# Kernel optimization log

Hardware: AMD Instinct MI355X
Metric: run time of the kernel (lower is better)

## Reference

```python
import jax, jax.numpy as jnp
import numpy as np

N, M, FDIM, EDIM, H, HEADS = 8192, 8192, 128, 128, 64, 4
NEG = -1e9


def setup_inputs() -> dict:
    key = jax.random.key(0)
    ks = jax.random.split(key, 6)
    F0 = jax.random.normal(ks[0], (N, FDIM), dtype=jnp.float32)
    E0 = jax.random.normal(ks[1], (M, EDIM), dtype=jnp.float32)
    A = jax.random.randint(ks[2], (N, M), 0, 2, dtype=jnp.int32)
    Wf = jax.random.normal(ks[3], (HEADS, FDIM, H), dtype=jnp.float32) * 0.05
    We = jax.random.normal(ks[4], (HEADS, EDIM, H), dtype=jnp.float32) * 0.05
    a = jax.random.normal(ks[5], (HEADS, H), dtype=jnp.float32) * 0.05
    return {"F0": F0, "E0": E0, "A": A, "Wf": Wf, "We": We, "a": a}


def reference(F0, E0, A, Wf, We, a):
    # Per-head linear projections: h=head, n/m=nodes, d=hidden
    F1 = jnp.einsum('nf,hfd->hnd', F0, Wf)   # [H, N, D]
    E1 = jnp.einsum('me,hed->hmd', E0, We)   # [H, M, D]
    # Additive GAT scores: (h_src @ a) + (h_dst @ a), broadcast over the grid
    e_src = jnp.einsum('hnd,hd->hn', F1, a)  # [H, N]
    e_dst = jnp.einsum('hmd,hd->hm', E1, a)  # [H, M]
    e = jax.nn.leaky_relu(e_src[:, :, None] + e_dst[:, None, :], negative_slope=0.2)
    e = jnp.where(A[None, :, :] > 0, e, NEG)
    alpha = jax.nn.softmax(e, axis=-1)       # [H, N, M]
    h_prime = jnp.einsum('hnm,hmd->hnd', alpha, E1)  # [H, N, D]
    out = jnp.mean(h_prime, axis=0)          # mean over heads -> [N, D]
    return jax.nn.softmax(out, axis=-1)
```

## Files before the change

### kernel.cpp

```cpp
#include <hip/hip_runtime.h>
#include <hip/hip_fp16.h>

#define NN 8192
#define MM 8192
#define FD 128
#define EDm 128
#define HD 64
#define NH 4
#define NTILE 32

typedef float f32x4 __attribute__((ext_vector_type(4)));
typedef _Float16 h16x8 __attribute__((ext_vector_type(8)));
typedef unsigned int u32;
typedef unsigned long long u64;

__global__ void k_esrc(const float* __restrict__ F0, const float* __restrict__ Wf,
                       const float* __restrict__ a, float* __restrict__ esrc) {
  __shared__ float vfL[NH * FD];
  int t = threadIdx.x;
#pragma unroll
  for (int r = 0; r < 2; ++r) {
    int idx = t + r * 256;
    int h = idx >> 7, f = idx & 127;
    const float* w = Wf + (size_t)(h * FD + f) * HD;
    const float* av = a + h * HD;
    float s = 0.f;
#pragma unroll
    for (int d = 0; d < HD; ++d) s += w[d] * av[d];
    vfL[idx] = s;
  }
  __syncthreads();
  int g = blockIdx.x * 256 + t;
  int n = g >> 2, h = g & 3;
  const float4* fr = (const float4*)(F0 + (size_t)n * FD);
  const float4* vr = (const float4*)(vfL + h * FD);
  float s = 0.f;
#pragma unroll
  for (int i = 0; i < FD / 4; ++i) {
    float4 x = fr[i], y = vr[i];
    s += x.x * y.x + x.y * y.y + x.z * y.z + x.w * y.w;
  }
  esrc[h * NN + n] = s;
}

__global__ void k_e1(const float* __restrict__ E0, const float* __restrict__ We,
                     const float* __restrict__ a, uint4* __restrict__ Bp,
                     _Float16* __restrict__ edh, _Float16* __restrict__ ed2h) {
  int wid = (blockIdx.x * blockDim.x + threadIdx.x) >> 6;
  int lane = threadIdx.x & 63;
  int h = wid >> 10;
  int mg = wid & 1023;
  int m = mg * 8;
  const float* we = We + (size_t)h * EDm * HD + lane;
  const float* e0r = E0 + (size_t)m * EDm;
  float ac[8] = {};
#pragma unroll 4
  for (int e = 0; e < EDm; ++e) {
    float wv = we[e * HD];
#pragma unroll
    for (int j = 0; j < 8; ++j) ac[j] += e0r[j * EDm + e] * wv;
  }
  int mc = mg >> 2, quad = mg & 3, dt = lane >> 4, col = lane & 15;
  union { h16x8 v; uint4 u; } hv;
#pragma unroll
  for (int j = 0; j < 8; ++j) hv.v[j] = (_Float16)ac[j];
  Bp[(((size_t)h * 256 + mc) * 4 + dt) * 64 + quad * 16 + col] = hv.u;

  float av = a[h * HD + lane];
  float d[8];
#pragma unroll
  for (int j = 0; j < 8; ++j) d[j] = ac[j] * av;
#pragma unroll
  for (int o = 32; o; o >>= 1)
#pragma unroll
    for (int j = 0; j < 8; ++j) d[j] += __shfl_xor(d[j], o);
  if (lane == 0) {
    const float L2E = 1.4426950408889634f;
    union { h16x8 v; uint4 u; } e1, e2;
#pragma unroll
    for (int j = 0; j < 8; ++j) {
      e1.v[j] = (_Float16)exp2f(d[j] * L2E);
      e2.v[j] = (_Float16)exp2f(0.2f * d[j] * L2E);
    }
    *(uint4*)(edh + (size_t)h * MM + m) = e1.u;
    *(uint4*)(ed2h + (size_t)h * MM + m) = e2.u;
  }
}

__global__ void k_pack(const int* __restrict__ A, u32* __restrict__ bitsG) {
  const int wid = (blockIdx.x * blockDim.x + threadIdx.x) >> 6;
  const int lane = threadIdx.x & 63;
  const int* ap = A + (size_t)wid * MM + lane;
  u32* op = bitsG + (size_t)wid * 256;
#pragma unroll 2
  for (int c = 0; c < 128; c += 8) {
    int v[8];
#pragma unroll
    for (int k = 0; k < 8; ++k)
      v[k] = __builtin_nontemporal_load(ap + (c + k) * 64);
    u64 b[8];
#pragma unroll
    for (int k = 0; k < 8; ++k) b[k] = __ballot(v[k] > 0);
    if (lane == 0) {
#pragma unroll
      for (int k = 0; k < 8; k += 2) {
        uint4 w = {(u32)b[k], (u32)(b[k] >> 32), (u32)b[k + 1], (u32)(b[k + 1] >> 32)};
        *(uint4*)(op + 2 * (c + k)) = w;
      }
    }
  }
}

__device__ __forceinline__ u32 hm2b(u32 w, int bit) {
  return (((w >> bit) & 1u) | (((w >> (bit + 1)) & 1u) << 16)) * 0xffffu;
}

__global__ __launch_bounds__(1024, 4) void k_main(
    const u32* __restrict__ bitsG, const uint4* __restrict__ Bp,
    const float* __restrict__ esrc, const _Float16* __restrict__ edh,
    const _Float16* __restrict__ ed2h, float* __restrict__ out) {
  __shared__ __align__(16) char smem[41472];
  u32* bits = (u32*)smem;
  float* Hsum = (float*)smem;
  float* Dsum = (float*)(smem + 32768);
  float* hp = (float*)(smem + 33280);

  const int t = threadIdx.x;
  const int lane = t & 63;
  const int wv = t >> 6;
  const int h = wv & 3;
  const int q = wv >> 2;
  const int col = lane & 15;
  const int quad = lane >> 4;
  const int qs = quad * 8;
  const int n0 = blockIdx.x * NTILE;
  const float L2E = 1.4426950408889634f;

#pragma unroll
  for (int i = 0; i < 2; ++i) {
    int tid = t + i * 1024;
    int row = tid >> 6, w4 = tid & 63;
    uint4 v = *(const uint4*)(bitsG + (size_t)(n0 + row) * 256 + w4 * 4);
    *(uint4*)(bits + row * 260 + w4 * 4) = v;
  }

  float s0 = esrc[h * NN + n0 + col];
  float s1 = esrc[h * NN + n0 + 16 + col];
  _Float16 e80 = (_Float16)exp2f(0.8f * s0 * L2E);
  _Float16 e81 = (_Float16)exp2f(0.8f * s1 * L2E);
  h16x8 es80 = {e80, e80, e80, e80, e80, e80, e80, e80};
  h16x8 es81 = {e81, e81, e81, e81, e81, e81, e81, e81};
  const h16x8 ones = {(_Float16)1.f, (_Float16)1.f, (_Float16)1.f, (_Float16)1.f,
                      (_Float16)1.f, (_Float16)1.f, (_Float16)1.f, (_Float16)1.f};

  const _Float16* edp = edh + (size_t)h * MM + qs;
  const _Float16* e2p = ed2h + (size_t)h * MM + qs;
  const uint4* bp = Bp + (size_t)h * 65536 + lane;

  uint4 b0s[2], b1s[2], b2s[2], b3s[2];
  h16x8 eds[2], e2s[2];
  u32 aw0s[2], aw1s[2];
#pragma unroll
  for (int i = 0; i < 2; ++i) {
    size_t w = (size_t)(q * 64 + i);
    b0s[i] = bp[w * 256];
    b1s[i] = bp[w * 256 + 64];
    b2s[i] = bp[w * 256 + 128];
    b3s[i] = bp[w * 256 + 192];
    eds[i] = *(const h16x8*)(edp + w * 32);
    e2s[i] = *(const h16x8*)(e2p + w * 32);
  }
  __syncthreads();

  const u32* rd0 = bits + col * 260 + q * 64;
  const u32* rd1 = bits + (col + 16) * 260 + q * 64;
  aw0s[0] = rd0[0]; aw1s[0] = rd1[0];
  aw0s[1] = rd0[1]; aw1s[1] = rd1[1];

  f32x4 acc[2][4] = {};
  f32x4 accd[2] = {};

#pragma unroll 2
  for (int it = 0; it < 64; ++it) {
    const int s = it & 1;
    const u32 aw0 = aw0s[s], aw1 = aw1s[s];
    union { h16x8 v; uint4 u; } w0, w1, b0, b1, b2, b3;
    b0.u = b0s[s]; b1.u = b1s[s]; b2.u = b2s[s]; b3.u = b3s[s];
    const h16x8 edv = eds[s], e2v = e2s[s];

    int ip = it + 2; if (ip > 63) ip = 63;
    const size_t wn = (size_t)(q * 64 + ip);
    b0s[s] = bp[wn * 256];
    b1s[s] = bp[wn * 256 + 64];
    b2s[s] = bp[wn * 256 + 128];
    b3s[s] = bp[wn * 256 + 192];
    eds[s] = *(const h16x8*)(edp + wn * 32);
    e2s[s] = *(const h16x8*)(e2p + wn * 32);
    aw0s[s] = rd0[ip];
    aw1s[s] = rd1[ip];

    uint4 m0, m1;
    m0.x = hm2b(aw0, qs);     m0.y = hm2b(aw0, qs + 2);
    m0.z = hm2b(aw0, qs + 4); m0.w = hm2b(aw0, qs + 6);
    m1.x = hm2b(aw1, qs);     m1.y = hm2b(aw1, qs + 2);
    m1.z = hm2b(aw1, qs + 4); m1.w = hm2b(aw1, qs + 6);

    w0.v = __builtin_elementwise_max(edv * es80, e2v);
    w1.v = __builtin_elementwise_max(edv * es81, e2v);
    w0.u.x &= m0.x; w0.u.y &= m0.y; w0.u.z &= m0.z; w0.u.w &= m0.w;
    w1.u.x &= m1.x; w1.u.y &= m1.y; w1.u.z &= m1.z; w1.u.w &= m1.w;

    acc[0][0] = __builtin_amdgcn_mfma_f32_16x16x32_f16(w0.v, b0.v, acc[0][0], 0, 0, 0);
    acc[1][0] = __builtin_amdgcn_mfma_f32_16x16x32_f16(w1.v, b0.v, acc[1][0], 0, 0, 0);
    acc[0][1] = __builtin_amdgcn_mfma_f32_16x16x32_f16(w0.v, b1.v, acc[0][1], 0, 0, 0);
    acc[1][1] = __builtin_amdgcn_mfma_f32_16x16x32_f16(w1.v, b1.v, acc[1][1], 0, 0, 0);
    acc[0][2] = __builtin_amdgcn_mfma_f32_16x16x32_f16(w0.v, b2.v, acc[0][2], 0, 0, 0);
    acc[1][2] = __builtin_amdgcn_mfma_f32_16x16x32_f16(w1.v, b2.v, acc[1][2], 0, 0, 0);
    acc[0][3] = __builtin_amdgcn_mfma_f32_16x16x32_f16(w0.v, b3.v, acc[0][3], 0, 0, 0);
    acc[1][3] = __builtin_amdgcn_mfma_f32_16x16x32_f16(w1.v, b3.v, acc[1][3], 0, 0, 0);
    accd[0] = __builtin_amdgcn_mfma_f32_16x16x32_f16(w0.v, ones, accd[0], 0, 0, 0);
    accd[1] = __builtin_amdgcn_mfma_f32_16x16x32_f16(w1.v, ones, accd[1], 0, 0, 0);
  }
  __syncthreads();

  for (int i = t; i < 8320; i += 1024) Hsum[i] = 0.f;
  __syncthreads();

  float* Hh = Hsum + h * 2048;
#pragma unroll
  for (int rt = 0; rt < 2; ++rt) {
#pragma unroll
    for (int dt = 0; dt < 4; ++dt)
#pragma unroll
      for (int r2 = 0; r2 < 4; ++r2)
        atomicAdd(&Hh[(rt * 16 + quad * 4 + r2) * 64 + dt * 16 + col],
                  acc[rt][dt][r2]);
    if (col == 0) {
#pragma unroll
      for (int r2 = 0; r2 < 4; ++r2)
        atomicAdd(&Dsum[h * 32 + rt * 16 + quad * 4 + r2], accd[rt][r2]);
    }
  }
  __syncthreads();

  for (int i = t; i < 2048; i += 1024) {
    int r = i >> 6;
    float v = 0.f;
#pragma unroll
    for (int hh = 0; hh < 4; ++hh) v += Hsum[hh * 2048 + i] / Dsum[hh * 32 + r];
    hp[i] = 0.25f * v;
  }
  __syncthreads();

#pragma unroll
  for (int i = 0; i < 2; ++i) {
    int r = wv * 2 + i;
    float v = hp[r * 64 + lane];
    float mx = v;
#pragma unroll
    for (int o = 32; o; o >>= 1) mx = fmaxf(mx, __shfl_xor(mx, o));
    float p = exp2f((v - mx) * L2E);
    float sm = p;
#pragma unroll
    for (int o = 32; o; o >>= 1) sm += __shfl_xor(sm, o);
    out[(size_t)(n0 + r) * HD + lane] = p / sm;
  }
}

extern "C" void kernel_launch(void* const* d_in, const int* in_sizes, int n_in,
                              void* d_out, int out_size, void* d_ws, size_t ws_size,
                              hipStream_t stream) {
  const float* F0 = (const float*)d_in[0];
  const float* E0 = (const float*)d_in[1];
  const int* A = (const int*)d_in[2];
  const float* Wf = (const float*)d_in[3];
  const float* We = (const float*)d_in[4];
  const float* a = (const float*)d_in[5];
  float* out = (float*)d_out;

  char* w = (char*)d_ws;
  float* esrc = (float*)w;        w += (size_t)NH * NN * 4;
  _Float16* edh = (_Float16*)w;   w += (size_t)NH * MM * 2;
  _Float16* ed2h = (_Float16*)w;  w += (size_t)NH * MM * 2;
  uint4* Bp = (uint4*)w;          w += (size_t)NH * HD * MM * 2;
  u32* bitsG = (u32*)w;           w += (size_t)NN * 256 * 4;

  k_pack<<<NN * 64 / 256, 256, 0, stream>>>(A, bitsG);
  k_esrc<<<(NH * NN) / 256, 256, 0, stream>>>(F0, Wf, a, esrc);
  k_e1<<<(NH * MM / 8) / 4, 256, 0, stream>>>(E0, We, a, Bp, edh, ed2h);
  k_main<<<NN / NTILE, 1024, 0, stream>>>(bitsG, Bp, esrc, edh, ed2h, out);
}
```

Measured before the change: 499.1 us.

## Split M across blocks with 128-row tiles, fuse prep kernels, add combine pass

```diff
diff --git a/kernel.cpp b/kernel.cpp
--- a/kernel.cpp
+++ b/kernel.cpp
@@ -7,106 +7,107 @@
 #define EDm 128
 #define HD 64
 #define NH 4
-#define NTILE 32
 
 typedef float f32x4 __attribute__((ext_vector_type(4)));
 typedef _Float16 h16x8 __attribute__((ext_vector_type(8)));
 typedef unsigned int u32;
 typedef unsigned long long u64;
 
-__global__ void k_esrc(const float* __restrict__ F0, const float* __restrict__ Wf,
-                       const float* __restrict__ a, float* __restrict__ esrc) {
+__global__ void k_prep(const int* __restrict__ A, u32* __restrict__ bitsG,
+                       const float* __restrict__ F0, const float* __restrict__ Wf,
+                       const float* __restrict__ aa, float* __restrict__ esrc,
+                       const float* __restrict__ E0, const float* __restrict__ We,
+                       uint4* __restrict__ Bp, _Float16* __restrict__ edh,
+                       _Float16* __restrict__ ed2h) {
   __shared__ float vfL[NH * FD];
-  int t = threadIdx.x;
-#pragma unroll
-  for (int r = 0; r < 2; ++r) {
-    int idx = t + r * 256;
-    int h = idx >> 7, f = idx & 127;
-    const float* w = Wf + (size_t)(h * FD + f) * HD;
-    const float* av = a + h * HD;
+  const int bid = blockIdx.x;
+  const int t = threadIdx.x;
+  const int lane = t & 63;
+
+  if (bid < 2048) {
+    const int row = bid * 4 + (t >> 6);
+    const int* ap = A + (size_t)row * MM + lane;
+    u32* op = bitsG + (size_t)row * 256;
+#pragma unroll 2
+    for (int c = 0; c < 128; c += 8) {
+      int v[8];
+#pragma unroll
+      for (int k = 0; k < 8; ++k)
+        v[k] = __builtin_nontemporal_load(ap + (c + k) * 64);
+      u64 b[8];
+#pragma unroll
+      for (int k = 0; k < 8; ++k) b[k] = __ballot(v[k] > 0);
+      if (lane == 0) {
+#pragma unroll
+        for (int k = 0; k < 8; k += 2) {
+          uint4 w = {(u32)b[k], (u32)(b[k] >> 32), (u32)b[k + 1], (u32)(b[k + 1] >> 32)};
+          *(uint4*)(op + 2 * (c + k)) = w;
+        }
+      }
+    }
+  } else if (bid < 2176) {
+    const int b2 = bid - 2048;
+#pragma unroll
+    for (int r = 0; r < 2; ++r) {
+      int idx = t + r * 256;
+      int h = idx >> 7, f = idx & 127;
+      const float* w = Wf + (size_t)(h * FD + f) * HD;
+      const float* av = aa + h * HD;
+      float s = 0.f;
+#pragma unroll
+      for (int d = 0; d < HD; ++d) s += w[d] * av[d];
+      vfL[idx] = s;
+    }
+    __syncthreads();
+    int g = b2 * 256 + t;
+    int n = g >> 2, h = g & 3;
+    const float4* fr = (const float4*)(F0 + (size_t)n * FD);
+    const float4* vr = (const float4*)(vfL + h * FD);
     float s = 0.f;
 #pragma unroll
-    for (int d = 0; d < HD; ++d) s += w[d] * av[d];
-    vfL[idx] = s;
-  }
-  __syncthreads();
-  int g = blockIdx.x * 256 + t;
-  int n = g >> 2, h = g & 3;
-  const float4* fr = (const float4*)(F0 + (size_t)n * FD);
-  const float4* vr = (const float4*)(vfL + h * FD);
-  float s = 0.f;
-#pragma unroll
-  for (int i = 0; i < FD / 4; ++i) {
-    float4 x = fr[i], y = vr[i];
-    s += x.x * y.x + x.y * y.y + x.z * y.z + x.w * y.w;
-  }
-  esrc[h * NN + n] = s;
-}
-
-__global__ void k_e1(const float* __restrict__ E0, const float* __restrict__ We,
-                     const float* __restrict__ a, uint4* __restrict__ Bp,
-                     _Float16* __restrict__ edh, _Float16* __restrict__ ed2h) {
-  int wid = (blockIdx.x * blockDim.x + threadIdx.x) >> 6;
-  int lane = threadIdx.x & 63;
-  int h = wid >> 10;
-  int mg = wid & 1023;
-  int m = mg * 8;
-  const float* we = We + (size_t)h * EDm * HD + lane;
-  const float* e0r = E0 + (size_t)m * EDm;
-  float ac[8] = {};
+    for (int i = 0; i < FD / 4; ++i) {
+      float4 x = fr[i], y = vr[i];
+      s += x.x * y.x + x.y * y.y + x.z * y.z + x.w * y.w;
+    }
+    esrc[h * NN + n] = s;
+  } else {
+    const int wid = (bid - 2176) * 4 + (t >> 6);
+    const int h = wid >> 10;
+    const int mg = wid & 1023;
+    const int m = mg * 8;
+    const float* we = We + (size_t)h * EDm * HD + lane;
+    const float* e0r = E0 + (size_t)m * EDm;
+    float ac[8] = {};
 #pragma unroll 4
-  for (int e = 0; e < EDm; ++e) {
-    float wv = we[e * HD];
-#pragma unroll
-    for (int j = 0; j < 8; ++j) ac[j] += e0r[j * EDm + e] * wv;
-  }
-  int mc = mg >> 2, quad = mg & 3, dt = lane >> 4, col = lane & 15;
-  union { h16x8 v; uint4 u; } hv;
-#pragma unroll
-  for (int j = 0; j < 8; ++j) hv.v[j] = (_Float16)ac[j];
-  Bp[(((size_t)h * 256 + mc) * 4 + dt) * 64 + quad * 16 + col] = hv.u;
-
-  float av = a[h * HD + lane];
-  float d[8];
-#pragma unroll
-  for (int j = 0; j < 8; ++j) d[j] = ac[j] * av;
-#pragma unroll
-  for (int o = 32; o; o >>= 1)
-#pragma unroll
-    for (int j = 0; j < 8; ++j) d[j] += __shfl_xor(d[j], o);
-  if (lane == 0) {
-    const float L2E = 1.4426950408889634f;
-    union { h16x8 v; uint4 u; } e1, e2;
-#pragma unroll
-    for (int j = 0; j < 8; ++j) {
-      e1.v[j] = (_Float16)exp2f(d[j] * L2E);
-      e2.v[j] = (_Float16)exp2f(0.2f * d[j] * L2E);
-    }
-    *(uint4*)(edh + (size_t)h * MM + m) = e1.u;
-    *(uint4*)(ed2h + (size_t)h * MM + m) = e2.u;
-  }
-}
-
-__global__ void k_pack(const int* __restrict__ A, u32* __restrict__ bitsG) {
-  const int wid = (blockIdx.x * blockDim.x + threadIdx.x) >> 6;
-  const int lane = threadIdx.x & 63;
-  const int* ap = A + (size_t)wid * MM + lane;
-  u32* op = bitsG + (size_t)wid * 256;
-#pragma unroll 2
-  for (int c = 0; c < 128; c += 8) {
-    int v[8];
-#pragma unroll
-    for (int k = 0; k < 8; ++k)
-      v[k] = __builtin_nontemporal_load(ap + (c + k) * 64);
-    u64 b[8];
-#pragma unroll
-    for (int k = 0; k < 8; ++k) b[k] = __ballot(v[k] > 0);
+    for (int e = 0; e < EDm; ++e) {
+      float wv = we[e * HD];
+#pragma unroll
+      for (int j = 0; j < 8; ++j) ac[j] += e0r[j * EDm + e] * wv;
+    }
+    int mc = mg >> 2, quad = mg & 3, dt = lane >> 4, col = lane & 15;
+    union { h16x8 v; uint4 u; } hv;
+#pragma unroll
+    for (int j = 0; j < 8; ++j) hv.v[j] = (_Float16)ac[j];
+    Bp[(((size_t)h * 256 + mc) * 4 + dt) * 64 + quad * 16 + col] = hv.u;
+
+    float av = aa[h * HD + lane];
+    float d[8];
+#pragma unroll
+    for (int j = 0; j < 8; ++j) d[j] = ac[j] * av;
+#pragma unroll
+    for (int o = 32; o; o >>= 1)
+#pragma unroll
+      for (int j = 0; j < 8; ++j) d[j] += __shfl_xor(d[j], o);
     if (lane == 0) {
-#pragma unroll
-      for (int k = 0; k < 8; k += 2) {
-        uint4 w = {(u32)b[k], (u32)(b[k] >> 32), (u32)b[k + 1], (u32)(b[k + 1] >> 32)};
-        *(uint4*)(op + 2 * (c + k)) = w;
+      const float L2E = 1.4426950408889634f;
+      union { h16x8 v; uint4 u; } e1, e2;
+#pragma unroll
+      for (int j = 0; j < 8; ++j) {
+        e1.v[j] = (_Float16)exp2f(d[j] * L2E);
+        e2.v[j] = (_Float16)exp2f(0.2f * d[j] * L2E);
       }
+      *(uint4*)(edh + (size_t)h * MM + m) = e1.u;
+      *(uint4*)(ed2h + (size_t)h * MM + m) = e2.u;
     }
   }
 }
@@ -118,34 +119,40 @@
 __global__ __launch_bounds__(1024, 4) void k_main(
     const u32* __restrict__ bitsG, const uint4* __restrict__ Bp,
     const float* __restrict__ esrc, const _Float16* __restrict__ edh,
-    const _Float16* __restrict__ ed2h, float* __restrict__ out) {
-  __shared__ __align__(16) char smem[41472];
-  u32* bits = (u32*)smem;
-  float* Hsum = (float*)smem;
-  float* Dsum = (float*)(smem + 32768);
-  float* hp = (float*)(smem + 33280);
+    const _Float16* __restrict__ ed2h, float* __restrict__ Npart,
+    float* __restrict__ Dpart) {
+  __shared__ __align__(16) u32 bits[128 * 68];
 
   const int t = threadIdx.x;
   const int lane = t & 63;
   const int wv = t >> 6;
   const int h = wv & 3;
-  const int q = wv >> 2;
+  const int g = wv >> 2;
   const int col = lane & 15;
   const int quad = lane >> 4;
   const int qs = quad * 8;
-  const int n0 = blockIdx.x * NTILE;
+  const int mq = blockIdx.x & 3;
+  const int n0 = (blockIdx.x >> 2) * 128;
   const float L2E = 1.4426950408889634f;
 
 #pragma unroll
   for (int i = 0; i < 2; ++i) {
-    int tid = t + i * 1024;
-    int row = tid >> 6, w4 = tid & 63;
-    uint4 v = *(const uint4*)(bitsG + (size_t)(n0 + row) * 256 + w4 * 4);
-    *(uint4*)(bits + row * 260 + w4 * 4) = v;
-  }
-
-  float s0 = esrc[h * NN + n0 + col];
-  float s1 = esrc[h * NN + n0 + 16 + col];
+    int idx = t + i * 1024;
+    int row = idx >> 4, u4 = idx & 15;
+    uint4 v = *(const uint4*)(bitsG + (size_t)(n0 + row) * 256 + mq * 64 + u4 * 4);
+    *(uint4*)(bits + row * 68 + u4 * 4) = v;
+  }
+
+  const uint4* bp = Bp + (size_t)h * 65536 + (size_t)mq * 64 * 256 + lane;
+  const _Float16* edp = edh + (size_t)h * MM + mq * 2048 + qs;
+  const _Float16* e2p = ed2h + (size_t)h * MM + mq * 2048 + qs;
+
+  uint4 bu0 = bp[0], bu1 = bp[64], bu2 = bp[128], bu3 = bp[192];
+  h16x8 edv = *(const h16x8*)edp;
+  h16x8 e2v = *(const h16x8*)e2p;
+
+  float s0 = esrc[h * NN + n0 + g * 32 + col];
+  float s1 = esrc[h * NN + n0 + g * 32 + 16 + col];
   _Float16 e80 = (_Float16)exp2f(0.8f * s0 * L2E);
   _Float16 e81 = (_Float16)exp2f(0.8f * s1 * L2E);
   h16x8 es80 = {e80, e80, e80, e80, e80, e80, e80, e80};
@@ -153,51 +160,25 @@
   const h16x8 ones = {(_Float16)1.f, (_Float16)1.f, (_Float16)1.f, (_Float16)1.f,
                       (_Float16)1.f, (_Float16)1.f, (_Float16)1.f, (_Float16)1.f};
 
-  const _Float16* edp = edh + (size_t)h * MM + qs;
-  const _Float16* e2p = ed2h + (size_t)h * MM + qs;
-  const uint4* bp = Bp + (size_t)h * 65536 + lane;
-
-  uint4 b0s[2], b1s[2], b2s[2], b3s[2];
-  h16x8 eds[2], e2s[2];
-  u32 aw0s[2], aw1s[2];
-#pragma unroll
-  for (int i = 0; i < 2; ++i) {
-    size_t w = (size_t)(q * 64 + i);
-    b0s[i] = bp[w * 256];
-    b1s[i] = bp[w * 256 + 64];
-    b2s[i] = bp[w * 256 + 128];
-    b3s[i] = bp[w * 256 + 192];
-    eds[i] = *(const h16x8*)(edp + w * 32);
-    e2s[i] = *(const h16x8*)(e2p + w * 32);
-  }
   __syncthreads();
 
-  const u32* rd0 = bits + col * 260 + q * 64;
-  const u32* rd1 = bits + (col + 16) * 260 + q * 64;
-  aw0s[0] = rd0[0]; aw1s[0] = rd1[0];
-  aw0s[1] = rd0[1]; aw1s[1] = rd1[1];
+  const u32* rd0 = bits + (g * 32 + col) * 68;
+  const u32* rd1 = bits + (g * 32 + 16 + col) * 68;
+  u32 aw0 = rd0[0], aw1 = rd1[0];
 
   f32x4 acc[2][4] = {};
   f32x4 accd[2] = {};
 
-#pragma unroll 2
   for (int it = 0; it < 64; ++it) {
-    const int s = it & 1;
-    const u32 aw0 = aw0s[s], aw1 = aw1s[s];
-    union { h16x8 v; uint4 u; } w0, w1, b0, b1, b2, b3;
-    b0.u = b0s[s]; b1.u = b1s[s]; b2.u = b2s[s]; b3.u = b3s[s];
-    const h16x8 edv = eds[s], e2v = e2s[s];
-
-    int ip = it + 2; if (ip > 63) ip = 63;
-    const size_t wn = (size_t)(q * 64 + ip);
-    b0s[s] = bp[wn * 256];
-    b1s[s] = bp[wn * 256 + 64];
-    b2s[s] = bp[wn * 256 + 128];
-    b3s[s] = bp[wn * 256 + 192];
-    eds[s] = *(const h16x8*)(edp + wn * 32);
-    e2s[s] = *(const h16x8*)(e2p + wn * 32);
-    aw0s[s] = rd0[ip];
-    aw1s[s] = rd1[ip];
+    const int ip = (it < 63) ? it + 1 : 63;
+    const u32 naw0 = rd0[ip];
+    const u32 naw1 = rd1[ip];
+    const uint4 nb0 = bp[ip * 256];
+    const uint4 nb1 = bp[ip * 256 + 64];
+    const uint4 nb2 = bp[ip * 256 + 128];
+    const uint4 nb3 = bp[ip * 256 + 192];
+    const h16x8 nedv = *(const h16x8*)(edp + ip * 32);
+    const h16x8 ne2v = *(const h16x8*)(e2p + ip * 32);
 
     uint4 m0, m1;
     m0.x = hm2b(aw0, qs);     m0.y = hm2b(aw0, qs + 2);
@@ -205,6 +186,8 @@
     m1.x = hm2b(aw1, qs);     m1.y = hm2b(aw1, qs + 2);
     m1.z = hm2b(aw1, qs + 4); m1.w = hm2b(aw1, qs + 6);
 
+    union { h16x8 v; uint4 u; } w0, w1, b0, b1, b2, b3;
+    b0.u = bu0; b1.u = bu1; b2.u = bu2; b3.u = bu3;
     w0.v = __builtin_elementwise_max(edv * es80, e2v);
     w1.v = __builtin_elementwise_max(edv * es81, e2v);
     w0.u.x &= m0.x; w0.u.y &= m0.y; w0.u.z &= m0.z; w0.u.w &= m0.w;
@@ -220,51 +203,58 @@
     acc[1][3] = __builtin_amdgcn_mfma_f32_16x16x32_f16(w1.v, b3.v, acc[1][3], 0, 0, 0);
     accd[0] = __builtin_amdgcn_mfma_f32_16x16x32_f16(w0.v, ones, accd[0], 0, 0, 0);
     accd[1] = __builtin_amdgcn_mfma_f32_16x16x32_f16(w1.v, ones, accd[1], 0, 0, 0);
-  }
-  __syncthreads();
-
-  for (int i = t; i < 8320; i += 1024) Hsum[i] = 0.f;
-  __syncthreads();
-
-  float* Hh = Hsum + h * 2048;
-#pragma unroll
-  for (int rt = 0; rt < 2; ++rt) {
+
+    aw0 = naw0; aw1 = naw1; edv = nedv; e2v = ne2v;
+    bu0 = nb0; bu1 = nb1; bu2 = nb2; bu3 = nb3;
+  }
+
+  float* np = Npart + (((size_t)(mq * 4 + h) * NN) + n0 + g * 32) * HD;
+#pragma unroll
+  for (int rt = 0; rt < 2; ++rt)
 #pragma unroll
     for (int dt = 0; dt < 4; ++dt)
 #pragma unroll
       for (int r2 = 0; r2 < 4; ++r2)
-        atomicAdd(&Hh[(rt * 16 + quad * 4 + r2) * 64 + dt * 16 + col],
-                  acc[rt][dt][r2]);
-    if (col == 0) {
+        np[(size_t)(rt * 16 + quad * 4 + r2) * HD + dt * 16 + col] = acc[rt][dt][r2];
+  if (col == 0) {
+    float* dp = Dpart + (size_t)(mq * 4 + h) * NN + n0 + g * 32;
+#pragma unroll
+    for (int rt = 0; rt < 2; ++rt)
 #pragma unroll
       for (int r2 = 0; r2 < 4; ++r2)
-        atomicAdd(&Dsum[h * 32 + rt * 16 + quad * 4 + r2], accd[rt][r2]);
-    }
-  }
-  __syncthreads();
-
-  for (int i = t; i < 2048; i += 1024) {
-    int r = i >> 6;
-    float v = 0.f;
-#pragma unroll
-    for (int hh = 0; hh < 4; ++hh) v += Hsum[hh * 2048 + i] / Dsum[hh * 32 + r];
-    hp[i] = 0.25f * v;
-  }
-  __syncthreads();
-
-#pragma unroll
-  for (int i = 0; i < 2; ++i) {
-    int r = wv * 2 + i;
-    float v = hp[r * 64 + lane];
-    float mx = v;
-#pragma unroll
-    for (int o = 32; o; o >>= 1) mx = fmaxf(mx, __shfl_xor(mx, o));
-    float p = exp2f((v - mx) * L2E);
-    float sm = p;
-#pragma unroll
-    for (int o = 32; o; o >>= 1) sm += __shfl_xor(sm, o);
-    out[(size_t)(n0 + r) * HD + lane] = p / sm;
-  }
+        dp[rt * 16 + quad * 4 + r2] = accd[rt][r2];
+  }
+}
+
+__global__ void k_comb(const float* __restrict__ Npart,
+                       const float* __restrict__ Dpart,
+                       float* __restrict__ out) {
+  const int t = threadIdx.x;
+  const int lane = t & 63;
+  const int n = blockIdx.x * 4 + (t >> 6);
+  const float L2E = 1.4426950408889634f;
+
+  float v = 0.f;
+#pragma unroll
+  for (int h = 0; h < NH; ++h) {
+    float num = 0.f, den = 0.f;
+#pragma unroll
+    for (int mq = 0; mq < 4; ++mq) {
+      num += Npart[(((size_t)(mq * 4 + h) * NN) + n) * HD + lane];
+      den += Dpart[(size_t)(mq * 4 + h) * NN + n];
+    }
+    v += num / den;
+  }
+  v *= 0.25f;
+
+  float mx = v;
+#pragma unroll
+  for (int o = 32; o; o >>= 1) mx = fmaxf(mx, __shfl_xor(mx, o));
+  float p = exp2f((v - mx) * L2E);
+  float sm = p;
+#pragma unroll
+  for (int o = 32; o; o >>= 1) sm += __shfl_xor(sm, o);
+  out[(size_t)n * HD + lane] = p / sm;
 }
 
 extern "C" void kernel_launch(void* const* d_in, const int* in_sizes, int n_in,
@@ -284,9 +274,10 @@
   _Float16* ed2h = (_Float16*)w;  w += (size_t)NH * MM * 2;
   uint4* Bp = (uint4*)w;          w += (size_t)NH * HD * MM * 2;
   u32* bitsG = (u32*)w;           w += (size_t)NN * 256 * 4;
-
-  k_pack<<<NN * 64 / 256, 256, 0, stream>>>(A, bitsG);
-  k_esrc<<<(NH * NN) / 256, 256, 0, stream>>>(F0, Wf, a, esrc);
-  k_e1<<<(NH * MM / 8) / 4, 256, 0, stream>>>(E0, We, a, Bp, edh, ed2h);
-  k_main<<<NN / NTILE, 1024, 0, stream>>>(bitsG, Bp, esrc, edh, ed2h, out);
-}
+  float* Npart = (float*)w;       w += (size_t)16 * NN * HD * 4;
+  float* Dpart = (float*)w;       w += (size_t)16 * NN * 4;
+
+  k_prep<<<3200, 256, 0, stream>>>(A, bitsG, F0, Wf, a, esrc, E0, We, Bp, edh, ed2h);
+  k_main<<<256, 1024, 0, stream>>>(bitsG, Bp, esrc, edh, ed2h, Npart, Dpart);
+  k_comb<<<NN / 4, 256, 0, stream>>>(Npart, Dpart, out);
+}
```

Measured after the change: 453.1 us. -9.2%, faster.
